# Optimization experiments

Hardware: AMD Instinct MI355X
Metric: run time of the kernel (lower is better)

The kernel has to match this reference:

```python
import jax, jax.numpy as jnp
import numpy as np

N, E, H, G, L = 50000, 640000, 128, 8, 3

def setup_inputs() -> dict:
    key = jax.random.key(0)
    ks = jax.random.split(key, 10)
    s = 1.0 / np.sqrt(H)
    return {
        "x": jax.random.normal(ks[0], (N, H), jnp.float32),
        "query": jax.random.normal(ks[1], (G, H), jnp.float32),
        "Wl": jax.random.normal(ks[2], (L, H, H), jnp.float32) * s,
        "bl": jax.random.normal(ks[3], (L, H), jnp.float32) * s,
        "Wr": jax.random.normal(ks[4], (L, H, H), jnp.float32) * s,
        "Wlin": jax.random.normal(ks[5], (H, H), jnp.float32) * s,
        "blin": jax.random.normal(ks[6], (H,), jnp.float32) * s,
        "edge_index": jax.random.randint(ks[7], (2, E), 0, N, jnp.int64),
        "batch_vec": jnp.sort(jax.random.randint(ks[8], (N,), 0, G, jnp.int64)),
    }

def reference(x, query, Wl, bl, Wr, Wlin, blin, edge_index, batch_vec):
    src, dst = edge_index[0], edge_index[1]
    n = x.shape[0]
    for i in range(L):
        # SAGEConv(aggr='max'): gather neighbor feats, scatter-max to dst
        m = jax.ops.segment_max(x[src], dst, num_segments=n)  # [N,H]
        m = jnp.where(jnp.isfinite(m), m, 0.0)  # isolated nodes -> 0 (PyG)
        x = jax.nn.relu(m @ Wl[i].T + bl[i] + x @ Wr[i].T)
    x = x @ Wlin.T + blin  # encoder final linear
    # cosine scoring per graph, vectorized via batch_vec
    xn = x / jnp.linalg.norm(x, axis=1, keepdims=True).clip(1e-12)
    qn = query / jnp.linalg.norm(query, axis=1, keepdims=True).clip(1e-12)
    scores = jnp.sum(xn * qn[batch_vec], axis=1)  # [N]
    return scores
```

## Files before the change

### kernel.cpp

```cpp
#include <hip/hip_runtime.h>
#include <math.h>

#define H 128
#define NBUCK_MAX 256

typedef _Float16 half8 __attribute__((ext_vector_type(8)));
typedef float f32x16 __attribute__((ext_vector_type(16)));
typedef int int4v __attribute__((ext_vector_type(4)));

__device__ __forceinline__ half8 h8max(half8 a, half8 b) {
#if defined(__has_builtin) && __has_builtin(__builtin_elementwise_max)
    return __builtin_elementwise_max(a, b);
#else
    half8 r;
#pragma unroll
    for (int j = 0; j < 8; ++j) r[j] = a[j] > b[j] ? a[j] : b[j];
    return r;
#endif
}

__device__ __forceinline__ half8 h8shfl_xor(half8 v, int mask) {
    int4v iv;
    __builtin_memcpy(&iv, &v, 16);
#pragma unroll
    for (int j = 0; j < 4; ++j) iv[j] = __shfl_xor(iv[j], mask, 64);
    half8 r;
    __builtin_memcpy(&r, &iv, 16);
    return r;
}


__global__ __launch_bounds__(256) void prep_all(
    const int* __restrict__ ei, int E, int* __restrict__ blockhist, int NB,
    const float* __restrict__ x, const float* __restrict__ query,
    const float* __restrict__ Wl, const float* __restrict__ Wr,
    const float* __restrict__ Wlin, _Float16* __restrict__ xh,
    _Float16* __restrict__ wimg, float* __restrict__ qn, int n8, int HB, int SB,
    int WB) {
    int b = blockIdx.x;
    int tid = threadIdx.x;
    if (b < HB) {
        __shared__ int hist[NBUCK_MAX];
        for (int j = tid; j < NB; j += 256) hist[j] = 0;
        __syncthreads();
        int base = b * 2048 + tid;
#pragma unroll
        for (int k = 0; k < 8; ++k) {
            int e = base + k * 256;
            if (e < E) atomicAdd(&hist[ei[E + e] >> 8], 1);
        }
        __syncthreads();
        for (int j = tid; j < NB; j += 256) blockhist[(size_t)b * NB + j] = hist[j];
    } else if (b < HB + SB) {
        int i = (b - HB) * 256 + tid;
        if (i < n8) {
            const float4* x4 = (const float4*)x;
            float4 u = x4[(size_t)i * 2], v = x4[(size_t)i * 2 + 1];
            float f[8] = {u.x, u.y, u.z, u.w, v.x, v.y, v.z, v.w};
            half8 h;
#pragma unroll
            for (int j = 0; j < 8; ++j) h[j] = (_Float16)f[j];
            *(half8*)(xh + (size_t)i * 8) = h;
        }
    } else if (b < HB + SB + WB) {
        int gidx = (b - HB - SB) * 256 + tid;
        if (gidx < 7 * 2048) {
            int mat = gidx / 2048;
            int rem = gidx - mat * 2048;
            int kc4 = rem >> 9;
            int r2 = rem & 511;
            int s = r2 >> 6;
            int lane = r2 & 63;
            int ks = s >> 2;
            int colgrp = s & 3;
            int lhi = lane >> 5, l31 = lane & 31;
            int n = colgrp * 32 + l31;
            int g16 = kc4 * 4 + ks * 2 + lhi;
            const float* src = (mat == 6) ? Wlin
                             : ((mat & 1) ? Wr + (mat >> 1) * H * H
                                          : Wl + (mat >> 1) * H * H);
            const float* p = src + n * H + g16 * 8;
            half8 h, l;
#pragma unroll
            for (int j = 0; j < 8; ++j) {
                float v = p[j];
                _Float16 hh = (_Float16)v;
                h[j] = hh;
                l[j] = (_Float16)(v - (float)hh);
            }
            size_t base = (size_t)mat * 32768 + (size_t)kc4 * 8192 +
                          (size_t)s * 1024 + (size_t)lane * 16;
            *(half8*)(wimg + base) = h;
            *(half8*)(wimg + base + 8) = l;
        }
    } else {
        int g = b - HB - SB - WB;
        __shared__ float part[4];
        float v = (tid < 128) ? query[g * H + tid] : 0.f;
        float ss = v * v;
#pragma unroll
        for (int off = 32; off > 0; off >>= 1) ss += __shfl_xor(ss, off, 64);
        if ((tid & 63) == 0) part[tid >> 6] = ss;
        __syncthreads();
        float tot = part[0] + part[1];
        if (tid < 128) qn[g * H + tid] = v / fmaxf(sqrtf(tot), 1e-12f);
    }
}


__global__ __launch_bounds__(512) void scan_hist(int* __restrict__ blockhist,
                                                 int HB, int NB,
                                                 int* __restrict__ coltot) {
    __shared__ int buf[512];
    int j = blockIdx.x;
    int tid = threadIdx.x;
    int carry = 0;
    for (int base = 0; base < HB; base += 512) {
        int t = base + tid;
        int v = (t < HB) ? blockhist[(size_t)t * NB + j] : 0;
        buf[tid] = v;
        __syncthreads();
        int incl = v;
#pragma unroll
        for (int off = 1; off < 512; off <<= 1) {
            int u = (tid >= off) ? buf[tid - off] : 0;
            __syncthreads();
            incl += u;
            buf[tid] = incl;
            __syncthreads();
        }
        if (t < HB) blockhist[(size_t)t * NB + j] = carry + incl - v;
        carry += buf[511];
        __syncthreads();
    }
    if (tid == 0) coltot[j] = carry;
}

__device__ __forceinline__ int lds_excl_scan256(const int* __restrict__ coltot,
                                                int NB, int* buf, int tid) {
    int v = (tid < NB) ? coltot[tid] : 0;
    buf[tid] = v;
    __syncthreads();
    int incl = v;
#pragma unroll
    for (int off = 1; off < 256; off <<= 1) {
        int u = (tid >= off) ? buf[tid - off] : 0;
        __syncthreads();
        incl += u;
        buf[tid] = incl;
        __syncthreads();
    }
    return incl - v;
}


__global__ __launch_bounds__(256) void scatter_edges(
    const int* __restrict__ ei, int E, const int* __restrict__ blockhist,
    const int* __restrict__ coltot, int NB, int2* __restrict__ bucketed) {
    __shared__ int sbuf[256];
    __shared__ int sbase[NBUCK_MAX];
    __shared__ int scnt[NBUCK_MAX];
    int b = blockIdx.x;
    int tid = threadIdx.x;
    int cs = lds_excl_scan256(coltot, NB, sbuf, tid);
    if (tid < NB) {
        sbase[tid] = cs + blockhist[(size_t)b * NB + tid];
        scnt[tid] = 0;
    }
    __syncthreads();
    int base = b * 2048 + tid;
#pragma unroll
    for (int k = 0; k < 8; ++k) {
        int e = base + k * 256;
        if (e < E) {
            int s = ei[e];
            int d = ei[E + e];
            int bu = d >> 8;
            int r = atomicAdd(&scnt[bu], 1);
            bucketed[sbase[bu] + r] = make_int2(d, s);
        }
    }
}


__global__ __launch_bounds__(256) void build_rows(
    const int2* __restrict__ bucketed, const int* __restrict__ coltot,
    int NB, int* __restrict__ deg, unsigned short* __restrict__ adjp16,
    int* __restrict__ govf, int* __restrict__ ovf, int N) {
    __shared__ int sbuf[256];
    __shared__ __align__(16) unsigned short rows[256 * 32];
    __shared__ int cnt[256];
    int k = blockIdx.x;
    int tid = threadIdx.x;
    int cs = lds_excl_scan256(coltot, NB, sbuf, tid);
    int s0 = __shfl(cs, 0, 64);
    if (tid == k % 256) sbuf[0] = cs;
    __syncthreads();
    if (tid == 0) {
        int acc = 0;
        for (int j = 0; j < k; ++j) acc += coltot[j];
        sbuf[0] = acc;
        sbuf[1] = coltot[k];
    }
    cnt[tid] = 0;
    for (int j = tid; j < 256 * 32; j += 256) rows[j] = 0;
    __syncthreads();
    s0 = sbuf[0];
    int cn = sbuf[1];

    for (int i = tid; i < cn; i += 256) {
        int2 rec = bucketed[s0 + i];
        int dl = rec.x & 255;
        int sl = atomicAdd(&cnt[dl], 1);
        if (sl < 32) {
            rows[dl * 32 + sl] = (unsigned short)rec.y;
        } else {
            int o = atomicAdd(govf, 1);
            ovf[2 * o] = rec.x;
            ovf[2 * o + 1] = rec.y;
        }
    }
    __syncthreads();
    int node0 = k << 8;
    if (node0 + tid < N) deg[node0 + tid] = cnt[tid];
    for (int j = tid; j < 1024; j += 256) {
        int row = j >> 2, q = j & 3;
        int node = node0 + row;
        if (node < N)
            ((int4*)adjp16)[(size_t)node * 4 + q] = ((const int4*)rows)[row * 4 + q];
    }
}


template <bool FINAL_UNUSED>
__global__ __launch_bounds__(512, 6) void layer_fused(
    const half8* __restrict__ Xh, const int* __restrict__ deg,
    const unsigned short* __restrict__ adjp16, const int* __restrict__ ovf,
    const int* __restrict__ ovfcnt, const _Float16* __restrict__ Bimg,
    const float* __restrict__ bias, _Float16* __restrict__ Yh, int N) {
    __shared__ __align__(16) unsigned char smem[16384];
    _Float16* sU = (_Float16*)smem;
    _Float16* sX = (_Float16*)(smem + 8192);
    float* comb = (float*)smem;

    int tid = threadIdx.x;
    int w = tid >> 6;
    int wq = w & 3;
    int wh = w >> 2;
    int lane = tid & 63;
    int l31 = lane & 31;
    int lhi = lane >> 5;
    int n0 = blockIdx.x * 32;

    const half8 hz = {(_Float16)0.f, (_Float16)0.f, (_Float16)0.f, (_Float16)0.f,
                      (_Float16)0.f, (_Float16)0.f, (_Float16)0.f, (_Float16)0.f};

    {
        int row = tid >> 4;
        int g = tid & 15;
        int nn = n0 + row;
        half8 h = hz;
        if (nn < N) h = Xh[(size_t)nn * 16 + g];
        *(half8*)&sX[row * 128 + ((g ^ (row & 15)) << 3)] = h;
    }

    {
        int sub = lane >> 4;
        int lf = lane & 15;
        int nd4 = n0 + w * 4;
        int node = nd4 + sub;
        int nodec = node < N ? node : N - 1;
        int degv = (node < N) ? deg[node] : 0;

        int dmx = degv;
        {
            int t = __shfl_xor(dmx, 16, 64);
            dmx = t > dmx ? t : dmx;
            t = __shfl_xor(dmx, 32, 64);
            dmx = t > dmx ? t : dmx;
        }

        int r0 = (int)adjp16[(size_t)nodec * 32 + lf];
        int r1 = 0;
        if (dmx > 16) r1 = (int)adjp16[(size_t)nodec * 32 + 16 + lf];
#pragma unroll
        for (int i = 0; i < 4; ++i) {
            int d = __shfl(degv, i << 4, 64);
            int base = i << 4;
            int j0 = sub, j1 = 4 + sub, j2 = 8 + sub, j3 = 12 + sub;
            int i0 = __shfl(r0, base | (j0 < d ? j0 : 0), 64);
            int i1 = __shfl(r0, base | (j1 < d ? j1 : 0), 64);
            int i2 = __shfl(r0, base | (j2 < d ? j2 : 0), 64);
            int i3 = __shfl(r0, base | (j3 < d ? j3 : 0), 64);
            half8 v0 = Xh[(size_t)i0 * 16 + lf];
            half8 v1 = Xh[(size_t)i1 * 16 + lf];
            half8 v2 = Xh[(size_t)i2 * 16 + lf];
            half8 v3 = Xh[(size_t)i3 * 16 + lf];
            half8 acc = h8max(h8max(v0, v1), h8max(v2, v3));
            if (d > 16) {
                int k4 = (16 + sub) < d ? sub : 0;
                int k5 = (20 + sub) < d ? 4 + sub : 0;
                int k6 = (24 + sub) < d ? 8 + sub : 0;
                int k7 = (28 + sub) < d ? 12 + sub : 0;
                int i4 = __shfl(r1, base | k4, 64);
                int i5 = __shfl(r1, base | k5, 64);
                int i6 = __shfl(r1, base | k6, 64);
                int i7 = __shfl(r1, base | k7, 64);
                half8 u0 = Xh[(size_t)i4 * 16 + lf];
                half8 u1 = Xh[(size_t)i5 * 16 + lf];
                half8 u2 = Xh[(size_t)i6 * 16 + lf];
                half8 u3 = Xh[(size_t)i7 * 16 + lf];
                acc = h8max(acc, h8max(h8max(u0, u1), h8max(u2, u3)));
            }
            if (d > 32) {
                int cntv = ovfcnt[0];
                for (int kk = 0; kk < cntv; ++kk) {
                    if (ovf[2 * kk] == nd4 + i) {
                        half8 u = Xh[(size_t)ovf[2 * kk + 1] * 16 + lf];
                        acc = h8max(acc, u);
                    }
                }
            }
            acc = h8max(acc, h8shfl_xor(acc, 16));
            acc = h8max(acc, h8shfl_xor(acc, 32));
            if (d == 0) acc = hz;
            int row = w * 4 + i;
            if (sub == 0) *(half8*)&sU[row * 128 + ((lf ^ (row & 15)) << 3)] = acc;
        }
    }
    __syncthreads();

    f32x16 acc;
    int col = wq * 32 + l31;
    {
        float b0 = (wh == 0) ? bias[col] : 0.f;
#pragma unroll
        for (int r = 0; r < 16; ++r) acc[r] = b0;
    }

    int rl = l31;
    const _Float16* A = wh ? sX : sU;
    const _Float16* B = Bimg + (size_t)wh * 32768;

#pragma unroll
    for (int kc4 = 0; kc4 < 4; ++kc4) {
#pragma unroll
        for (int ks = 0; ks < 2; ++ks) {
            int g16 = kc4 * 4 + ks * 2 + lhi;
            int posA = g16 ^ (rl & 15);
            half8 ah = *(const half8*)&A[rl * 128 + posA * 8];
            size_t boff =
                (size_t)kc4 * 8192 + (size_t)(ks * 4 + wq) * 1024 + (size_t)lane * 16;
            half8 bh = *(const half8*)&B[boff];
            half8 bl2 = *(const half8*)&B[boff + 8];
            acc = __builtin_amdgcn_mfma_f32_32x32x16_f16(ah, bh, acc, 0, 0, 0);
            acc = __builtin_amdgcn_mfma_f32_32x32x16_f16(ah, bl2, acc, 0, 0, 0);
        }
    }

    __syncthreads();

    if (wh == 1) {
#pragma unroll
        for (int r = 0; r < 16; ++r) {
            int rloc = (r & 3) + 8 * (r >> 2) + 4 * lhi;
            comb[wq * 1024 + rloc * 32 + l31] = acc[r];
        }
    }
    __syncthreads();

    if (wh == 0) {
#pragma unroll
        for (int r = 0; r < 16; ++r) {
            int rloc = (r & 3) + 8 * (r >> 2) + 4 * lhi;
            float y = acc[r] + comb[wq * 1024 + rloc * 32 + l31];
            int row = n0 + rloc;
            if (row < N) Yh[(size_t)row * H + col] = (_Float16)fmaxf(y, 0.f);
        }
    }
}


__global__ __launch_bounds__(256) void final_mfma6(
    const half8* __restrict__ Xh, const _Float16* __restrict__ Bimg,
    const float* __restrict__ blin, const float* __restrict__ qn,
    const int* __restrict__ bv, float* __restrict__ out, int N) {
    __shared__ __align__(16) _Float16 sA[4096];

    int tid = threadIdx.x;
    int w = tid >> 6;
    int lane = tid & 63;
    int l31 = lane & 31;
    int lhi = lane >> 5;
    int n0 = blockIdx.x * 32;

    {
        const half8 hz = {(_Float16)0.f, (_Float16)0.f, (_Float16)0.f, (_Float16)0.f,
                          (_Float16)0.f, (_Float16)0.f, (_Float16)0.f, (_Float16)0.f};
#pragma unroll
        for (int t = 0; t < 2; ++t) {
            int idx = tid + t * 256;
            int row = idx >> 4;
            int g = idx & 15;
            int nn = n0 + row;
            half8 h = hz;
            if (nn < N) h = Xh[(size_t)nn * 16 + g];
            *(half8*)&sA[row * 128 + ((g ^ (row & 15)) << 3)] = h;
        }
    }

    int arow = n0 + l31;
    arow = arow < N ? arow : N - 1;
    int gl = bv[arow];

    f32x16 acc;
    int col = w * 32 + l31;
    {
        float b = blin[col];
#pragma unroll
        for (int r = 0; r < 16; ++r) acc[r] = b;
    }
    int rl = l31;
    __syncthreads();

#pragma unroll
    for (int kc4 = 0; kc4 < 4; ++kc4) {
#pragma unroll
        for (int ks = 0; ks < 2; ++ks) {
            int g16 = kc4 * 4 + ks * 2 + lhi;
            int posA = g16 ^ (rl & 15);
            half8 ah = *(const half8*)&sA[rl * 128 + posA * 8];
            size_t boff =
                (size_t)kc4 * 8192 + (size_t)(ks * 4 + w) * 1024 + (size_t)lane * 16;
            half8 bh = *(const half8*)&Bimg[boff];
            half8 bl2 = *(const half8*)&Bimg[boff + 8];
            acc = __builtin_amdgcn_mfma_f32_32x32x16_f16(ah, bh, acc, 0, 0, 0);
            acc = __builtin_amdgcn_mfma_f32_32x32x16_f16(ah, bl2, acc, 0, 0, 0);
        }
    }

    __syncthreads();
    float* sP = (float*)sA;
#pragma unroll
    for (int r = 0; r < 16; ++r) {
        int rloc = (r & 3) + 8 * (r >> 2) + 4 * lhi;
        int g = __shfl(gl, rloc, 32);
        float y = acc[r];
        float q = qn[(size_t)g * H + col];
        float ss = y * y;
        float sd = y * q;
#pragma unroll
        for (int off = 1; off <= 16; off <<= 1) {
            ss += __shfl_xor(ss, off, 64);
            sd += __shfl_xor(sd, off, 64);
        }
        if (l31 == 0) {
            sP[(rloc * 4 + w) * 2] = ss;
            sP[(rloc * 4 + w) * 2 + 1] = sd;
        }
    }
    __syncthreads();
    if (tid < 32) {
        int row = n0 + tid;
        if (row < N) {
            float ss = 0.f, sd = 0.f;
#pragma unroll
            for (int q = 0; q < 4; ++q) {
                ss += sP[(tid * 4 + q) * 2];
                sd += sP[(tid * 4 + q) * 2 + 1];
            }
            out[row] = sd / fmaxf(sqrtf(ss), 1e-12f);
        }
    }
}


extern "C" void kernel_launch(void* const* d_in, const int* in_sizes, int n_in,
                              void* d_out, int out_size, void* d_ws, size_t ws_size,
                              hipStream_t stream) {
    const float* x = (const float*)d_in[0];
    const float* query = (const float*)d_in[1];
    const float* Wl = (const float*)d_in[2];
    const float* bl = (const float*)d_in[3];
    const float* Wr = (const float*)d_in[4];
    const float* Wlin = (const float*)d_in[5];
    const float* blin = (const float*)d_in[6];
    const int* ei = (const int*)d_in[7];
    const int* bv = (const int*)d_in[8];
    float* out = (float*)d_out;

    const int N = in_sizes[0] / H;
    const int E = in_sizes[7] / 2;
    const int G = in_sizes[1] / H;

    const int HB = (E + 2047) / 2048;
    const int NB = (N + 255) >> 8;

    char* p = (char*)d_ws;
    auto alloc = [&](size_t bytes) {
        char* r = p;
        p += (bytes + 255) & ~(size_t)255;
        return r;
    };
    int* deg = (int*)alloc((size_t)(N + 1) * sizeof(int));
    int* govf = deg + N;
    unsigned short* adjp16 =
        (unsigned short*)alloc((size_t)N * 32 * sizeof(unsigned short));
    int* ovf = (int*)alloc((size_t)E * 2 * sizeof(int));
    int* blockhist = (int*)alloc((size_t)HB * NB * sizeof(int));
    int* coltot = (int*)alloc((size_t)NB * sizeof(int));
    int2* bucketed = (int2*)alloc((size_t)E * sizeof(int2));
    float* qn = (float*)alloc((size_t)G * H * sizeof(float));
    _Float16* wimg = (_Float16*)alloc((size_t)7 * 32768 * sizeof(_Float16));
    size_t actH = (size_t)N * H * sizeof(_Float16);
    _Float16* xah = (_Float16*)alloc(actH);
    _Float16* xbh = (_Float16*)alloc(actH);

    hipMemsetAsync(govf, 0, sizeof(int), stream);

    const int n8 = N * H / 8;
    const int SB = (n8 + 255) / 256;
    const int WB = (7 * 2048 + 255) / 256;
    prep_all<<<HB + SB + WB + G, 256, 0, stream>>>(ei, E, blockhist, NB, x,
                                                   query, Wl, Wr, Wlin, xah,
                                                   wimg, qn, n8, HB, SB, WB);
    scan_hist<<<NB, 512, 0, stream>>>(blockhist, HB, NB, coltot);
    scatter_edges<<<HB, 256, 0, stream>>>(ei, E, blockhist, coltot, NB,
                                          bucketed);
    build_rows<<<NB, 256, 0, stream>>>(bucketed, coltot, NB, deg, adjp16, govf,
                                       ovf, N);

    const int NGm = (N + 31) / 32;

    layer_fused<false><<<NGm, 512, 0, stream>>>(
        (const half8*)xah, deg, adjp16, ovf, govf, wimg + (size_t)0 * 65536,
        bl + 0 * H, xbh, N);
    layer_fused<false><<<NGm, 512, 0, stream>>>(
        (const half8*)xbh, deg, adjp16, ovf, govf, wimg + (size_t)1 * 65536,
        bl + 1 * H, xah, N);
    layer_fused<false><<<NGm, 512, 0, stream>>>(
        (const half8*)xah, deg, adjp16, ovf, govf, wimg + (size_t)2 * 65536,
        bl + 2 * H, xbh, N);
    final_mfma6<<<NGm, 256, 0, stream>>>(
        (const half8*)xbh, wimg + (size_t)6 * 32768, blin, qn, bv, out, N);
}
```

Baseline: 233.2 us.

## Process 64 nodes per block in layer kernel with per-wave full-K MFMA

The fused SAGE layer now handles 64 rows per 512-thread block instead of 32. Each wave computes a 32-row tile over both the aggregated (Wl) and self (Wr) operands sequentially, rather than splitting K across wave halves and reducing through LDS, which removes two barriers and the LDS combine. Each wave's gather now covers 8 nodes instead of 4 using two adjacency registers. build_rows also takes its segment offsets from the inclusive LDS scan instead of a serial per-block loop. LDS use doubles to 32KB and the grid is halved, which may lower occupancy.

```diff
diff --git a/kernel.cpp b/kernel.cpp
--- a/kernel.cpp
+++ b/kernel.cpp
@@ -136,8 +136,8 @@
     if (tid == 0) coltot[j] = carry;
 }
 
-__device__ __forceinline__ int lds_excl_scan256(const int* __restrict__ coltot,
-                                                int NB, int* buf, int tid) {
+__device__ __forceinline__ int lds_scan256(const int* __restrict__ coltot,
+                                           int NB, int* buf, int tid) {
     int v = (tid < NB) ? coltot[tid] : 0;
     buf[tid] = v;
     __syncthreads();
@@ -162,7 +162,7 @@
     __shared__ int scnt[NBUCK_MAX];
     int b = blockIdx.x;
     int tid = threadIdx.x;
-    int cs = lds_excl_scan256(coltot, NB, sbuf, tid);
+    int cs = lds_scan256(coltot, NB, sbuf, tid);
     if (tid < NB) {
         sbase[tid] = cs + blockhist[(size_t)b * NB + tid];
         scnt[tid] = 0;
@@ -192,21 +192,12 @@
     __shared__ int cnt[256];
     int k = blockIdx.x;
     int tid = threadIdx.x;
-    int cs = lds_excl_scan256(coltot, NB, sbuf, tid);
-    int s0 = __shfl(cs, 0, 64);
-    if (tid == k % 256) sbuf[0] = cs;
-    __syncthreads();
-    if (tid == 0) {
-        int acc = 0;
-        for (int j = 0; j < k; ++j) acc += coltot[j];
-        sbuf[0] = acc;
-        sbuf[1] = coltot[k];
-    }
+    (void)lds_scan256(coltot, NB, sbuf, tid);
     cnt[tid] = 0;
     for (int j = tid; j < 256 * 32; j += 256) rows[j] = 0;
     __syncthreads();
-    s0 = sbuf[0];
-    int cn = sbuf[1];
+    int s0 = (k > 0) ? sbuf[k - 1] : 0;
+    int cn = sbuf[k] - s0;
 
     for (int i = tid; i < cn; i += 256) {
         int2 rec = bucketed[s0 + i];
@@ -238,26 +229,26 @@
     const unsigned short* __restrict__ adjp16, const int* __restrict__ ovf,
     const int* __restrict__ ovfcnt, const _Float16* __restrict__ Bimg,
     const float* __restrict__ bias, _Float16* __restrict__ Yh, int N) {
-    __shared__ __align__(16) unsigned char smem[16384];
-    _Float16* sU = (_Float16*)smem;
-    _Float16* sX = (_Float16*)(smem + 8192);
-    float* comb = (float*)smem;
+    __shared__ __align__(16) _Float16 sU[8192];
+    __shared__ __align__(16) _Float16 sX[8192];
 
     int tid = threadIdx.x;
     int w = tid >> 6;
     int wq = w & 3;
-    int wh = w >> 2;
+    int wr = w >> 2;
     int lane = tid & 63;
     int l31 = lane & 31;
     int lhi = lane >> 5;
-    int n0 = blockIdx.x * 32;
+    int n0 = blockIdx.x * 64;
 
     const half8 hz = {(_Float16)0.f, (_Float16)0.f, (_Float16)0.f, (_Float16)0.f,
                       (_Float16)0.f, (_Float16)0.f, (_Float16)0.f, (_Float16)0.f};
 
-    {
-        int row = tid >> 4;
-        int g = tid & 15;
+#pragma unroll
+    for (int t = 0; t < 2; ++t) {
+        int idx = tid + t * 512;
+        int row = idx >> 4;
+        int g = idx & 15;
         int nn = n0 + row;
         half8 h = hz;
         if (nn < N) h = Xh[(size_t)nn * 16 + g];
@@ -267,31 +258,42 @@
     {
         int sub = lane >> 4;
         int lf = lane & 15;
-        int nd4 = n0 + w * 4;
-        int node = nd4 + sub;
-        int nodec = node < N ? node : N - 1;
-        int degv = (node < N) ? deg[node] : 0;
+        int nd8 = n0 + w * 8;
+        int nn = nd8 + (lane & 7);
+        int degv = (nn < N) ? deg[nn] : 0;
 
         int dmx = degv;
+#pragma unroll
+        for (int off = 1; off <= 4; off <<= 1) {
+            int t = __shfl_xor(dmx, off, 64);
+            dmx = t > dmx ? t : dmx;
+        }
         {
-            int t = __shfl_xor(dmx, 16, 64);
+            int t = __shfl_xor(dmx, 8, 64);
             dmx = t > dmx ? t : dmx;
-            t = __shfl_xor(dmx, 32, 64);
-            dmx = t > dmx ? t : dmx;
-        }
-
-        int r0 = (int)adjp16[(size_t)nodec * 32 + lf];
-        int r1 = 0;
-        if (dmx > 16) r1 = (int)adjp16[(size_t)nodec * 32 + 16 + lf];
-#pragma unroll
-        for (int i = 0; i < 4; ++i) {
-            int d = __shfl(degv, i << 4, 64);
-            int base = i << 4;
+        }
+
+        int c0 = nd8 + (lane >> 4);
+        c0 = c0 < N ? c0 : N - 1;
+        int c1 = nd8 + 4 + (lane >> 4);
+        c1 = c1 < N ? c1 : N - 1;
+        int lf16 = lane & 15;
+        int r0 = (int)adjp16[(size_t)c0 * 32 + lf16];
+        int r1 = (int)adjp16[(size_t)c1 * 32 + lf16];
+        int r2 = 0, r3 = 0;
+        if (dmx > 16) {
+            r2 = (int)adjp16[(size_t)c0 * 32 + 16 + lf16];
+            r3 = (int)adjp16[(size_t)c1 * 32 + 16 + lf16];
+        }
+#pragma unroll
+        for (int i = 0; i < 8; ++i) {
+            int d = __shfl(degv, i, 64);
+            int base = (i & 3) << 4;
             int j0 = sub, j1 = 4 + sub, j2 = 8 + sub, j3 = 12 + sub;
-            int i0 = __shfl(r0, base | (j0 < d ? j0 : 0), 64);
-            int i1 = __shfl(r0, base | (j1 < d ? j1 : 0), 64);
-            int i2 = __shfl(r0, base | (j2 < d ? j2 : 0), 64);
-            int i3 = __shfl(r0, base | (j3 < d ? j3 : 0), 64);
+            int i0 = __shfl(i < 4 ? r0 : r1, base | (j0 < d ? j0 : 0), 64);
+            int i1 = __shfl(i < 4 ? r0 : r1, base | (j1 < d ? j1 : 0), 64);
+            int i2 = __shfl(i < 4 ? r0 : r1, base | (j2 < d ? j2 : 0), 64);
+            int i3 = __shfl(i < 4 ? r0 : r1, base | (j3 < d ? j3 : 0), 64);
             half8 v0 = Xh[(size_t)i0 * 16 + lf];
             half8 v1 = Xh[(size_t)i1 * 16 + lf];
             half8 v2 = Xh[(size_t)i2 * 16 + lf];
@@ -302,10 +304,10 @@
                 int k5 = (20 + sub) < d ? 4 + sub : 0;
                 int k6 = (24 + sub) < d ? 8 + sub : 0;
                 int k7 = (28 + sub) < d ? 12 + sub : 0;
-                int i4 = __shfl(r1, base | k4, 64);
-                int i5 = __shfl(r1, base | k5, 64);
-                int i6 = __shfl(r1, base | k6, 64);
-                int i7 = __shfl(r1, base | k7, 64);
+                int i4 = __shfl(i < 4 ? r2 : r3, base | k4, 64);
+                int i5 = __shfl(i < 4 ? r2 : r3, base | k5, 64);
+                int i6 = __shfl(i < 4 ? r2 : r3, base | k6, 64);
+                int i7 = __shfl(i < 4 ? r2 : r3, base | k7, 64);
                 half8 u0 = Xh[(size_t)i4 * 16 + lf];
                 half8 u1 = Xh[(size_t)i5 * 16 + lf];
                 half8 u2 = Xh[(size_t)i6 * 16 + lf];
@@ -315,7 +317,7 @@
             if (d > 32) {
                 int cntv = ovfcnt[0];
                 for (int kk = 0; kk < cntv; ++kk) {
-                    if (ovf[2 * kk] == nd4 + i) {
+                    if (ovf[2 * kk] == nd8 + i) {
                         half8 u = Xh[(size_t)ovf[2 * kk + 1] * 16 + lf];
                         acc = h8max(acc, u);
                     }
@@ -324,7 +326,7 @@
             acc = h8max(acc, h8shfl_xor(acc, 16));
             acc = h8max(acc, h8shfl_xor(acc, 32));
             if (d == 0) acc = hz;
-            int row = w * 4 + i;
+            int row = w * 8 + i;
             if (sub == 0) *(half8*)&sU[row * 128 + ((lf ^ (row & 15)) << 3)] = acc;
         }
     }
@@ -333,14 +335,12 @@
     f32x16 acc;
     int col = wq * 32 + l31;
     {
-        float b0 = (wh == 0) ? bias[col] : 0.f;
+        float b0 = bias[col];
 #pragma unroll
         for (int r = 0; r < 16; ++r) acc[r] = b0;
     }
 
-    int rl = l31;
-    const _Float16* A = wh ? sX : sU;
-    const _Float16* B = Bimg + (size_t)wh * 32768;
+    int rl = wr * 32 + l31;
 
 #pragma unroll
     for (int kc4 = 0; kc4 < 4; ++kc4) {
@@ -348,35 +348,37 @@
         for (int ks = 0; ks < 2; ++ks) {
             int g16 = kc4 * 4 + ks * 2 + lhi;
             int posA = g16 ^ (rl & 15);
-            half8 ah = *(const half8*)&A[rl * 128 + posA * 8];
+            half8 ah = *(const half8*)&sU[rl * 128 + posA * 8];
             size_t boff =
                 (size_t)kc4 * 8192 + (size_t)(ks * 4 + wq) * 1024 + (size_t)lane * 16;
-            half8 bh = *(const half8*)&B[boff];
-            half8 bl2 = *(const half8*)&B[boff + 8];
+            half8 bh = *(const half8*)&Bimg[boff];
+            half8 bl2 = *(const half8*)&Bimg[boff + 8];
             acc = __builtin_amdgcn_mfma_f32_32x32x16_f16(ah, bh, acc, 0, 0, 0);
             acc = __builtin_amdgcn_mfma_f32_32x32x16_f16(ah, bl2, acc, 0, 0, 0);
         }
     }
 
-    __syncthreads();
-
-    if (wh == 1) {
-#pragma unroll
-        for (int r = 0; r < 16; ++r) {
-            int rloc = (r & 3) + 8 * (r >> 2) + 4 * lhi;
-            comb[wq * 1024 + rloc * 32 + l31] = acc[r];
-        }
-    }
-    __syncthreads();
-
-    if (wh == 0) {
-#pragma unroll
-        for (int r = 0; r < 16; ++r) {
-            int rloc = (r & 3) + 8 * (r >> 2) + 4 * lhi;
-            float y = acc[r] + comb[wq * 1024 + rloc * 32 + l31];
-            int row = n0 + rloc;
-            if (row < N) Yh[(size_t)row * H + col] = (_Float16)fmaxf(y, 0.f);
-        }
+    const _Float16* Br = Bimg + 32768;
+#pragma unroll
+    for (int kc4 = 0; kc4 < 4; ++kc4) {
+#pragma unroll
+        for (int ks = 0; ks < 2; ++ks) {
+            int g16 = kc4 * 4 + ks * 2 + lhi;
+            int posA = g16 ^ (rl & 15);
+            half8 ah = *(const half8*)&sX[rl * 128 + posA * 8];
+            size_t boff =
+                (size_t)kc4 * 8192 + (size_t)(ks * 4 + wq) * 1024 + (size_t)lane * 16;
+            half8 bh = *(const half8*)&Br[boff];
+            half8 bl2 = *(const half8*)&Br[boff + 8];
+            acc = __builtin_amdgcn_mfma_f32_32x32x16_f16(ah, bh, acc, 0, 0, 0);
+            acc = __builtin_amdgcn_mfma_f32_32x32x16_f16(ah, bl2, acc, 0, 0, 0);
+        }
+    }
+
+#pragma unroll
+    for (int r = 0; r < 16; ++r) {
+        int row = n0 + wr * 32 + (r & 3) + 8 * (r >> 2) + 4 * lhi;
+        if (row < N) Yh[(size_t)row * H + col] = (_Float16)fmaxf(acc[r], 0.f);
     }
 }
 
@@ -530,7 +532,8 @@
     build_rows<<<NB, 256, 0, stream>>>(bucketed, coltot, NB, deg, adjp16, govf,
                                        ovf, N);
 
-    const int NGm = (N + 31) / 32;
+    const int NGm = (N + 63) / 64;
+    const int NGf = (N + 31) / 32;
 
     layer_fused<false><<<NGm, 512, 0, stream>>>(
         (const half8*)xah, deg, adjp16, ovf, govf, wimg + (size_t)0 * 65536,
@@ -541,6 +544,6 @@
     layer_fused<false><<<NGm, 512, 0, stream>>>(
         (const half8*)xah, deg, adjp16, ovf, govf, wimg + (size_t)2 * 65536,
         bl + 2 * H, xbh, N);
-    final_mfma6<<<NGm, 256, 0, stream>>>(
+    final_mfma6<<<NGf, 256, 0, stream>>>(
         (const half8*)xbh, wimg + (size_t)6 * 32768, blin, qn, bv, out, N);
 }
```

Result: no change. 237.1 us (+1.6%).

## Merge edge-sort kernels into one cooperative kernel with grid syncs

Applied to the files above, without the earlier changes.

Replaces the histogram, column scan, scatter and row-build kernels plus the memset with a single cooperative launch that separates the phases with grid.sync(). The aim is to remove several kernel launch gaps and the host memset. The scan now uses 256-thread blocks instead of 512, and the histogram work no longer shares a launch with the x/weight conversion in prep_all. The cooperative launch needs all HB (~313) blocks to be co-resident, and grid syncs carry their own cost.

```diff
diff --git a/kernel.cpp b/kernel.cpp
--- a/kernel.cpp
+++ b/kernel.cpp
@@ -1,8 +1,11 @@
 #include <hip/hip_runtime.h>
+#include <hip/hip_cooperative_groups.h>
 #include <math.h>
 
 #define H 128
 #define NBUCK_MAX 256
+
+namespace cg = cooperative_groups;
 
 typedef _Float16 half8 __attribute__((ext_vector_type(8)));
 typedef float f32x16 __attribute__((ext_vector_type(16)));
@@ -31,28 +34,15 @@
 
 
 __global__ __launch_bounds__(256) void prep_all(
-    const int* __restrict__ ei, int E, int* __restrict__ blockhist, int NB,
     const float* __restrict__ x, const float* __restrict__ query,
     const float* __restrict__ Wl, const float* __restrict__ Wr,
     const float* __restrict__ Wlin, _Float16* __restrict__ xh,
-    _Float16* __restrict__ wimg, float* __restrict__ qn, int n8, int HB, int SB,
+    _Float16* __restrict__ wimg, float* __restrict__ qn, int n8, int SB,
     int WB) {
     int b = blockIdx.x;
     int tid = threadIdx.x;
-    if (b < HB) {
-        __shared__ int hist[NBUCK_MAX];
-        for (int j = tid; j < NB; j += 256) hist[j] = 0;
-        __syncthreads();
-        int base = b * 2048 + tid;
-#pragma unroll
-        for (int k = 0; k < 8; ++k) {
-            int e = base + k * 256;
-            if (e < E) atomicAdd(&hist[ei[E + e] >> 8], 1);
-        }
-        __syncthreads();
-        for (int j = tid; j < NB; j += 256) blockhist[(size_t)b * NB + j] = hist[j];
-    } else if (b < HB + SB) {
-        int i = (b - HB) * 256 + tid;
+    if (b < SB) {
+        int i = b * 256 + tid;
         if (i < n8) {
             const float4* x4 = (const float4*)x;
             float4 u = x4[(size_t)i * 2], v = x4[(size_t)i * 2 + 1];
@@ -62,8 +52,8 @@
             for (int j = 0; j < 8; ++j) h[j] = (_Float16)f[j];
             *(half8*)(xh + (size_t)i * 8) = h;
         }
-    } else if (b < HB + SB + WB) {
-        int gidx = (b - HB - SB) * 256 + tid;
+    } else if (b < SB + WB) {
+        int gidx = (b - SB) * 256 + tid;
         if (gidx < 7 * 2048) {
             int mat = gidx / 2048;
             int rem = gidx - mat * 2048;
@@ -94,7 +84,7 @@
             *(half8*)(wimg + base + 8) = l;
         }
     } else {
-        int g = b - HB - SB - WB;
+        int g = b - SB - WB;
         __shared__ float part[4];
         float v = (tid < 128) ? query[g * H + tid] : 0.f;
         float ss = v * v;
@@ -107,37 +97,8 @@
     }
 }
 
-
-__global__ __launch_bounds__(512) void scan_hist(int* __restrict__ blockhist,
-                                                 int HB, int NB,
-                                                 int* __restrict__ coltot) {
-    __shared__ int buf[512];
-    int j = blockIdx.x;
-    int tid = threadIdx.x;
-    int carry = 0;
-    for (int base = 0; base < HB; base += 512) {
-        int t = base + tid;
-        int v = (t < HB) ? blockhist[(size_t)t * NB + j] : 0;
-        buf[tid] = v;
-        __syncthreads();
-        int incl = v;
-#pragma unroll
-        for (int off = 1; off < 512; off <<= 1) {
-            int u = (tid >= off) ? buf[tid - off] : 0;
-            __syncthreads();
-            incl += u;
-            buf[tid] = incl;
-            __syncthreads();
-        }
-        if (t < HB) blockhist[(size_t)t * NB + j] = carry + incl - v;
-        carry += buf[511];
-        __syncthreads();
-    }
-    if (tid == 0) coltot[j] = carry;
-}
-
-__device__ __forceinline__ int lds_excl_scan256(const int* __restrict__ coltot,
-                                                int NB, int* buf, int tid) {
+__device__ __forceinline__ int lds_scan256(const int* __restrict__ coltot,
+                                           int NB, int* buf, int tid) {
     int v = (tid < NB) ? coltot[tid] : 0;
     buf[tid] = v;
     __syncthreads();
@@ -154,80 +115,112 @@
 }
 
 
-__global__ __launch_bounds__(256) void scatter_edges(
-    const int* __restrict__ ei, int E, const int* __restrict__ blockhist,
-    const int* __restrict__ coltot, int NB, int2* __restrict__ bucketed) {
-    __shared__ int sbuf[256];
-    __shared__ int sbase[NBUCK_MAX];
-    __shared__ int scnt[NBUCK_MAX];
+__global__ __launch_bounds__(256) void coop_sort(
+    const int* __restrict__ ei, int E, int* __restrict__ blockhist, int HB,
+    int NB, int* __restrict__ coltot, int2* __restrict__ bucketed,
+    int* __restrict__ deg, unsigned short* __restrict__ adjp16,
+    int* __restrict__ govf, int* __restrict__ ovf, int N) {
+    cg::grid_group grid = cg::this_grid();
+    __shared__ __align__(16) unsigned char smem[18688];
+    int* sbuf = (int*)smem;
     int b = blockIdx.x;
     int tid = threadIdx.x;
-    int cs = lds_excl_scan256(coltot, NB, sbuf, tid);
-    if (tid < NB) {
-        sbase[tid] = cs + blockhist[(size_t)b * NB + tid];
-        scnt[tid] = 0;
-    }
-    __syncthreads();
-    int base = b * 2048 + tid;
-#pragma unroll
-    for (int k = 0; k < 8; ++k) {
-        int e = base + k * 256;
-        if (e < E) {
-            int s = ei[e];
-            int d = ei[E + e];
-            int bu = d >> 8;
-            int r = atomicAdd(&scnt[bu], 1);
-            bucketed[sbase[bu] + r] = make_int2(d, s);
-        }
-    }
-}
-
-
-__global__ __launch_bounds__(256) void build_rows(
-    const int2* __restrict__ bucketed, const int* __restrict__ coltot,
-    int NB, int* __restrict__ deg, unsigned short* __restrict__ adjp16,
-    int* __restrict__ govf, int* __restrict__ ovf, int N) {
-    __shared__ int sbuf[256];
-    __shared__ __align__(16) unsigned short rows[256 * 32];
-    __shared__ int cnt[256];
-    int k = blockIdx.x;
-    int tid = threadIdx.x;
-    int cs = lds_excl_scan256(coltot, NB, sbuf, tid);
-    int s0 = __shfl(cs, 0, 64);
-    if (tid == k % 256) sbuf[0] = cs;
-    __syncthreads();
-    if (tid == 0) {
-        int acc = 0;
-        for (int j = 0; j < k; ++j) acc += coltot[j];
-        sbuf[0] = acc;
-        sbuf[1] = coltot[k];
-    }
-    cnt[tid] = 0;
-    for (int j = tid; j < 256 * 32; j += 256) rows[j] = 0;
-    __syncthreads();
-    s0 = sbuf[0];
-    int cn = sbuf[1];
-
-    for (int i = tid; i < cn; i += 256) {
-        int2 rec = bucketed[s0 + i];
-        int dl = rec.x & 255;
-        int sl = atomicAdd(&cnt[dl], 1);
-        if (sl < 32) {
-            rows[dl * 32 + sl] = (unsigned short)rec.y;
-        } else {
-            int o = atomicAdd(govf, 1);
-            ovf[2 * o] = rec.x;
-            ovf[2 * o + 1] = rec.y;
-        }
-    }
-    __syncthreads();
-    int node0 = k << 8;
-    if (node0 + tid < N) deg[node0 + tid] = cnt[tid];
-    for (int j = tid; j < 1024; j += 256) {
-        int row = j >> 2, q = j & 3;
-        int node = node0 + row;
-        if (node < N)
-            ((int4*)adjp16)[(size_t)node * 4 + q] = ((const int4*)rows)[row * 4 + q];
+
+    {
+        if (b == 0 && tid == 0) *govf = 0;
+        for (int j = tid; j < NB; j += 256) sbuf[j] = 0;
+        __syncthreads();
+        int base = b * 2048 + tid;
+#pragma unroll
+        for (int k = 0; k < 8; ++k) {
+            int e = base + k * 256;
+            if (e < E) atomicAdd(&sbuf[ei[E + e] >> 8], 1);
+        }
+        __syncthreads();
+        for (int j = tid; j < NB; j += 256)
+            blockhist[(size_t)b * NB + j] = sbuf[j];
+    }
+    grid.sync();
+
+    if (b < NB) {
+        int carry = 0;
+        for (int base = 0; base < HB; base += 256) {
+            int t = base + tid;
+            int v = (t < HB) ? blockhist[(size_t)t * NB + b] : 0;
+            sbuf[tid] = v;
+            __syncthreads();
+            int incl = v;
+#pragma unroll
+            for (int off = 1; off < 256; off <<= 1) {
+                int u = (tid >= off) ? sbuf[tid - off] : 0;
+                __syncthreads();
+                incl += u;
+                sbuf[tid] = incl;
+                __syncthreads();
+            }
+            if (t < HB) blockhist[(size_t)t * NB + b] = carry + incl - v;
+            carry += sbuf[255];
+            __syncthreads();
+        }
+        if (tid == 0) coltot[b] = carry;
+    }
+    grid.sync();
+
+    {
+        int* sbase = (int*)(smem + 1024);
+        int* scnt = (int*)(smem + 2048);
+        int cs = lds_scan256(coltot, NB, sbuf, tid);
+        if (tid < NB) {
+            sbase[tid] = cs + blockhist[(size_t)b * NB + tid];
+            scnt[tid] = 0;
+        }
+        __syncthreads();
+        int base = b * 2048 + tid;
+#pragma unroll
+        for (int k = 0; k < 8; ++k) {
+            int e = base + k * 256;
+            if (e < E) {
+                int s = ei[e];
+                int d = ei[E + e];
+                int bu = d >> 8;
+                int r = atomicAdd(&scnt[bu], 1);
+                bucketed[sbase[bu] + r] = make_int2(d, s);
+            }
+        }
+    }
+    grid.sync();
+
+    if (b < NB) {
+        unsigned short* rows = (unsigned short*)(smem + 1024);
+        int* cnt = (int*)(smem + 17408);
+        (void)lds_scan256(coltot, NB, sbuf, tid);
+        cnt[tid] = 0;
+        for (int j = tid; j < 256 * 32; j += 256) rows[j] = 0;
+        __syncthreads();
+        int s0 = (b > 0) ? sbuf[b - 1] : 0;
+        int cn = sbuf[b] - s0;
+        for (int i = tid; i < cn; i += 256) {
+            int2 rec = bucketed[s0 + i];
+            int dl = rec.x & 255;
+            int sl = atomicAdd(&cnt[dl], 1);
+            if (sl < 32) {
+                rows[dl * 32 + sl] = (unsigned short)rec.y;
+            } else {
+                int o = atomicAdd(govf, 1);
+                ovf[2 * o] = rec.x;
+                ovf[2 * o + 1] = rec.y;
+            }
+        }
+        __syncthreads();
+        int node0 = b << 8;
+        if (node0 + tid < N) deg[node0 + tid] = cnt[tid];
+        for (int j = tid; j < 1024; j += 256) {
+            int row = j >> 2, q = j & 3;
+            int node = node0 + row;
+            if (node < N)
+                ((int4*)adjp16)[(size_t)node * 4 + q] =
+                    ((const int4*)rows)[row * 4 + q];
+        }
     }
 }
 
@@ -516,19 +509,27 @@
     _Float16* xah = (_Float16*)alloc(actH);
     _Float16* xbh = (_Float16*)alloc(actH);
 
-    hipMemsetAsync(govf, 0, sizeof(int), stream);
-
     const int n8 = N * H / 8;
     const int SB = (n8 + 255) / 256;
     const int WB = (7 * 2048 + 255) / 256;
-    prep_all<<<HB + SB + WB + G, 256, 0, stream>>>(ei, E, blockhist, NB, x,
-                                                   query, Wl, Wr, Wlin, xah,
-                                                   wimg, qn, n8, HB, SB, WB);
-    scan_hist<<<NB, 512, 0, stream>>>(blockhist, HB, NB, coltot);
-    scatter_edges<<<HB, 256, 0, stream>>>(ei, E, blockhist, coltot, NB,
-                                          bucketed);
-    build_rows<<<NB, 256, 0, stream>>>(bucketed, coltot, NB, deg, adjp16, govf,
-                                       ovf, N);
+    prep_all<<<SB + WB + G, 256, 0, stream>>>(x, query, Wl, Wr, Wlin, xah,
+                                              wimg, qn, n8, SB, WB);
+
+    {
+        int Ev = E, HBv = HB, NBv = NB, Nv = N;
+        const int* eiv = ei;
+        int* bhv = blockhist;
+        int* ctv = coltot;
+        int2* bkv = bucketed;
+        int* degv = deg;
+        unsigned short* adjv = adjp16;
+        int* gov = govf;
+        int* ovv = ovf;
+        void* kargs[] = {&eiv, &Ev, &bhv, &HBv, &NBv, &ctv,
+                         &bkv, &degv, &adjv, &gov, &ovv, &Nv};
+        hipLaunchCooperativeKernel((void*)coop_sort, dim3(HB), dim3(256), kargs,
+                                   0, stream);
+    }
 
     const int NGm = (N + 31) / 32;
 
```

Result: slower. 354.8 us (+52.1%).
